# Optimization experiments

Measured on AMD Instinct MI355X. Metric: run time of the kernel, lower is better.

Reference implementation:

```python
import jax, jax.numpy as jnp
import numpy as np

B, P, D, N, H = 1, 256, 512, 8, 64
STD = 0.02
IGNORE = -1000000.0


def setup_inputs() -> dict:
    key = jax.random.key(0)
    ks = jax.random.split(key, 9)
    inp = {"normalized_resid_pre": jax.random.normal(ks[0], (B, P, D), jnp.float32)}
    for i, s in enumerate("ABCDE"):
        inp["W_" + s] = STD * jax.random.normal(ks[i + 1], (N, D, H), jnp.float32)
        inp["b_" + s] = jnp.zeros((N, H), jnp.float32)
    inp["W_V"] = STD * jax.random.normal(ks[6], (N, H, H, H), jnp.float32)
    inp["W_K"] = STD * jax.random.normal(ks[7], (N, H, H, H), jnp.float32)
    inp["W_O"] = STD * jax.random.normal(ks[8], (N, H, D), jnp.float32)
    inp["b_O"] = jnp.zeros((D,), jnp.float32)
    return inp


def reference(normalized_resid_pre, W_A, b_A, W_B, b_B, W_C, b_C, W_D, b_D, W_E, b_E, W_V, W_K, W_O, b_O):
    x = normalized_resid_pre
    b_sz = x.shape[0]
    proj = lambda W, b: jnp.einsum('ndh,bpd->bpnh', W, x) + b
    ta = proj(W_A, b_A)
    tb = proj(W_B, b_B)
    tc = proj(W_C, b_C)
    td = proj(W_D, b_D)
    te = proj(W_E, b_E)
    # V_Layer: v[b, p1, p2, n, h3]
    v = jnp.einsum('bpnh,bqng,nhgf->bpqnf', td, te, W_V)
    # TrittentionCScore: chained einsums -> scores[b, n, p, q, r]
    step1 = jnp.einsum('brnk,nijk->brij', tc, W_K)
    step2 = jnp.einsum('brij,bqnj->briq', step1, tb)
    scores = jnp.einsum('briq,bpni->bnpqr', step2, ta)
    # CausalMask (attn_eq=False, order_attn=True): mask over (t=p, s=q, q=r) dims
    ti = jnp.arange(P)[:, None, None]
    si = jnp.arange(P)[None, :, None]
    qi = jnp.arange(P)[None, None, :]
    mask = (ti >= qi) | (si >= qi) | (ti >= si)  # [P, P, P]
    scores = jnp.where(mask, IGNORE, scores)
    # TrittentionCPattern: b n p q r -> b n r (p q), /d_head, extra column, softmax
    flat = jnp.transpose(scores, (0, 1, 4, 2, 3)).reshape(b_sz, N, P, P * P) / H
    extra = jnp.full((b_sz, N, P, 1), -1000.0, flat.dtype)
    attn = jax.nn.softmax(jnp.concatenate([flat, extra], axis=-1), axis=-1)
    # Z_Layer: v -> b n h (p s), extra zero column, combine
    vf = jnp.transpose(v, (0, 3, 4, 1, 2)).reshape(b_sz, N, H, P * P)
    vf = jnp.concatenate([vf, jnp.zeros((b_sz, N, H, 1), vf.dtype)], axis=-1)
    z = jnp.einsum('bnql,bnhl->bqnh', attn, vf)
    # Result + Out
    zint = jnp.einsum('bqnh,nhd->bqnd', z, W_O)
    return zint.sum(axis=2) + b_O
```

## Files before the change

kernel.cpp:

```cpp
#include <hip/hip_runtime.h>
#include <hip/hip_bf16.h>


typedef __hip_bfloat16 bf16;
typedef __attribute__((ext_vector_type(8))) short short8;
typedef __attribute__((ext_vector_type(4))) short s16x4;
typedef __attribute__((ext_vector_type(4))) float floatx4;

__device__ __forceinline__ float ldf(const float* p){ return *p; }
__device__ __forceinline__ float ldf(const bf16* p){ return __bfloat162float(*p); }
__device__ __forceinline__ void  stf(float* p, float v){ *p = v; }
__device__ __forceinline__ void  stf(bf16*  p, float v){ *p = __float2bfloat16(v); }

__device__ __forceinline__ floatx4 mfma16(short8 a, short8 b, floatx4 c){
  return __builtin_amdgcn_mfma_f32_16x16x32_bf16(a, b, c, 0, 0, 0);
}
__device__ __forceinline__ short8 ld_g8(const bf16* p){
  return *reinterpret_cast<const short8*>(p);
}
__device__ __forceinline__ short bfs(float x){
  bf16 v = __float2bfloat16(x);
  return *reinterpret_cast<short*>(&v);
}

__device__ __forceinline__ void ld4(const bf16* p, float* o){
  s16x4 v = *reinterpret_cast<const s16x4*>(p);
  #pragma unroll
  for (int i = 0; i < 4; i++)
    o[i] = __uint_as_float(((unsigned)(unsigned short)v[i]) << 16);
}
__device__ __forceinline__ void ld4(const float* p, float* o){
  float4 v = *reinterpret_cast<const float4*>(p);
  o[0] = v.x; o[1] = v.y; o[2] = v.z; o[3] = v.w;
}

__device__ __forceinline__ bool is_bf16_x(const void* xv)
{
  const unsigned* x32 = (const unsigned*)xv;
  unsigned w = x32[threadIdx.x & 63];
  unsigned lo = w & 0xFFFFu;
  unsigned e  = (lo >> 7) & 0xFFu;
  bool v = (lo == 0u) || (e >= 90u && e <= 145u);
  unsigned long long m = __ballot(v);
  return __popcll(m) >= 40;
}

template<typename TI>
__device__ __forceinline__ void proj_body(
    const TI* __restrict__ x, const TI* const* Ws, const TI* const* bs,
    bf16* __restrict__ tproj, float* As, float* Bs)
{
  const int bz = blockIdx.z, j = bz >> 3, n = bz & 7;
  const TI* B    = Ws[j] + (size_t)n * 32768;
  const TI* bias = bs[j] + n * 64;
  bf16* out = tproj + (size_t)j * 131072;
  const int m0 = blockIdx.y * 64;
  const int t = threadIdx.x, tx = t & 15, ty = t >> 4;
  float acc[4][4] = {};
  for (int k0 = 0; k0 < 512; k0 += 16) {
    { int m = t >> 2, kk = (t & 3) * 4;
      float a[4]; ld4(x + (size_t)(m0 + m) * 512 + (k0 + kk), a);
      As[(kk+0)*68+m] = a[0]; As[(kk+1)*68+m] = a[1];
      As[(kk+2)*68+m] = a[2]; As[(kk+3)*68+m] = a[3]; }
    { int kk = t >> 4, nn = (t & 15) * 4;
      float b[4]; ld4(B + (size_t)(k0 + kk) * 64 + nn, b);
      Bs[kk*68+nn+0] = b[0]; Bs[kk*68+nn+1] = b[1];
      Bs[kk*68+nn+2] = b[2]; Bs[kk*68+nn+3] = b[3]; }
    __syncthreads();
    #pragma unroll
    for (int kk = 0; kk < 16; kk++) {
      float4 a4 = *reinterpret_cast<const float4*>(&As[kk*68 + ty*4]);
      float4 b4 = *reinterpret_cast<const float4*>(&Bs[kk*68 + tx*4]);
      float av[4] = {a4.x,a4.y,a4.z,a4.w}, bv[4] = {b4.x,b4.y,b4.z,b4.w};
      #pragma unroll
      for (int im = 0; im < 4; im++)
        #pragma unroll
        for (int in = 0; in < 4; in++) acc[im][in] += av[im] * bv[in];
    }
    __syncthreads();
  }
  #pragma unroll
  for (int im = 0; im < 4; im++)
    #pragma unroll
    for (int in = 0; in < 4; in++) {
      float v = acc[im][in] + ldf(bias + tx*4 + in);
      int p = m0 + ty*4 + im, h = tx*4 + in;
      if (j < 3) out[(size_t)p * 512 + n*64 + h] = __float2bfloat16(v);
      else       out[(size_t)n * 16384 + (size_t)h * 256 + p] = __float2bfloat16(v);
    }
}

__global__ __launch_bounds__(256) void proj_all(
    const void* __restrict__ x,
    const void* W0, const void* b0, const void* W1, const void* b1,
    const void* W2, const void* b2, const void* W3, const void* b3,
    const void* W4, const void* b4, bf16* __restrict__ tproj)
{
  __shared__ float As[16*68];
  __shared__ float Bs[16*68];
  if (is_bf16_x(x)) {
    const bf16* Ws[5] = {(const bf16*)W0,(const bf16*)W1,(const bf16*)W2,
                         (const bf16*)W3,(const bf16*)W4};
    const bf16* bs[5] = {(const bf16*)b0,(const bf16*)b1,(const bf16*)b2,
                         (const bf16*)b3,(const bf16*)b4};
    proj_body<bf16>((const bf16*)x, Ws, bs, tproj, As, Bs);
  } else {
    const float* Ws[5] = {(const float*)W0,(const float*)W1,(const float*)W2,
                          (const float*)W3,(const float*)W4};
    const float* bs[5] = {(const float*)b0,(const float*)b1,(const float*)b2,
                          (const float*)b3,(const float*)b4};
    proj_body<float>((const float*)x, Ws, bs, tproj, As, Bs);
  }
}

template<typename TW>
__device__ __forceinline__ void s1t_body(
    const bf16* __restrict__ tc, const TW* __restrict__ WK,
    bf16* __restrict__ s1t)
{
  const int i = blockIdx.x;
  const int t = threadIdx.x, wid = t >> 6, lane = t & 63, quad = lane >> 4, l16 = lane & 15;
  const int rw = blockIdx.y * 64 + wid * 16;
  floatx4 acc[4];
  #pragma unroll
  for (int jt = 0; jt < 4; jt++) acc[jt] = (floatx4){0.f, 0.f, 0.f, 0.f};
  for (int kc = 0; kc < 16; kc++) {
    short8 af = ld_g8(tc + (size_t)(rw + l16) * 512 + kc*32 + quad*8);
    const int n = kc >> 1, kk = (kc & 1) * 32 + quad * 8;
    #pragma unroll
    for (int jt = 0; jt < 4; jt++) {
      const TW* bp = WK + ((size_t)(n*64 + i) * 64 + jt*16 + l16) * 64 + kk;
      short8 bf;
      if constexpr (sizeof(TW) == 2) {
        bf = ld_g8((const bf16*)bp);
      } else {
        float4 x0 = *reinterpret_cast<const float4*>(bp);
        float4 x1 = *reinterpret_cast<const float4*>(bp + 4);
        bf[0]=bfs(x0.x); bf[1]=bfs(x0.y); bf[2]=bfs(x0.z); bf[3]=bfs(x0.w);
        bf[4]=bfs(x1.x); bf[5]=bfs(x1.y); bf[6]=bfs(x1.z); bf[7]=bfs(x1.w);
      }
      acc[jt] = mfma16(af, bf, acc[jt]);
    }
  }
  #pragma unroll
  for (int jt = 0; jt < 4; jt++)
    #pragma unroll
    for (int reg = 0; reg < 4; reg++)
      s1t[(size_t)(rw + quad*4 + reg) * 4096 + i*64 + jt*16 + l16] =
          __float2bfloat16(acc[jt][reg]);
}

__global__ __launch_bounds__(256) void s1t_all(
    const void* __restrict__ x, const bf16* __restrict__ tb,
    const bf16* __restrict__ tc, const void* __restrict__ WK,
    bf16* __restrict__ tbsbf, bf16* __restrict__ s1t)
{
  if (blockIdx.y == 4) {
    int t = blockIdx.x * 256 + threadIdx.x;
    int q = t >> 6, j = t & 63;
    float s = 0.f;
    #pragma unroll
    for (int n = 0; n < 8; n++) s += ldf(tb + q*512 + n*64 + j);
    tbsbf[t] = __float2bfloat16(s * 0.015625f);
    return;
  }
  if (is_bf16_x(x)) s1t_body<bf16>(tc, (const bf16*)WK, s1t);
  else              s1t_body<float>(tc, (const float*)WK, s1t);
}

#define E_PHASE(PT, BUF)                                                      \
  {                                                                           \
    const int ptb_ = ((PT)*4 + wid) * 16;                                     \
    for (int qt2 = 0; qt2 < 2; qt2++) {                                       \
      const int qh = qc + qt2*16;                                             \
      char* erow0 = (BUF) + (quad*4)*72 + (qt2*16 + l16)*2;                   \
      if (qh + 15 <= ptb_) {                                                  \
        for (int reg = 0; reg < 4; reg++)                                     \
          *reinterpret_cast<bf16*>(erow0 + reg*72) = __float2bfloat16(0.f);   \
      } else {                                                                \
        floatx4 acc = {0.f, 0.f, 0.f, 0.f};                                   \
        acc = mfma16(taf[PT][0], cfr[qt2][0], acc);                           \
        acc = mfma16(taf[PT][1], cfr[qt2][1], acc);                           \
        if (qh >= ptb_ + 16 && qh + 15 < r) {                                 \
          for (int reg = 0; reg < 4; reg++) {                                 \
            float e = __expf(acc[reg]);                                       \
            Zp += e;                                                          \
            *reinterpret_cast<bf16*>(erow0 + reg*72) = __float2bfloat16(e);   \
          }                                                                   \
        } else {                                                              \
          for (int reg = 0; reg < 4; reg++) {                                 \
            int p = ptb_ + quad*4 + reg;                                      \
            int q = qh + l16;                                                 \
            float e = (p < q && q < r) ? __expf(acc[reg]) : 0.f;              \
            Zp += e;                                                          \
            *reinterpret_cast<bf16*>(erow0 + reg*72) = __float2bfloat16(e);   \
          }                                                                   \
        }                                                                     \
      }                                                                       \
    }                                                                         \
  }

__global__ __launch_bounds__(256) void tri_attn(
    const bf16* __restrict__ ta,
    const bf16* __restrict__ tbsbf,
    const bf16* __restrict__ s1t,
    const bf16* __restrict__ tdT,
    const bf16* __restrict__ teT,
    bf16* __restrict__ Sbuf)
{
  __shared__ __align__(16) char smb[44544];
  const int bx = blockIdx.x;
  const int n = bx & 7;
  const int r = 255 - (bx >> 3);
  const int t = threadIdx.x;
  const int wid = t >> 6, lane = t & 63, quad = lane >> 4, l16 = lane & 15;
  bf16* srow = Sbuf + (size_t)n * 1048576 + (size_t)r * 4096;
  if (r < 2) {
    short8 zz = (short8){0,0,0,0,0,0,0,0};
    reinterpret_cast<short8*>(srow)[t]       = zz;
    reinterpret_cast<short8*>(srow)[t + 256] = zz;
    return;
  }
  const int nch  = ((r - 1) >> 5) + 1;
  const int rcap = nch * 32;

  {
    const bf16* s1r = s1t + (size_t)r * 4096;
    short8 bfr[4][2];
    #pragma unroll
    for (int it = 0; it < 4; it++)
      #pragma unroll
      for (int kc = 0; kc < 2; kc++)
        bfr[it][kc] = ld_g8(s1r + (it*16 + l16)*64 + kc*32 + quad*8);
    #pragma unroll
    for (int qt = 0; qt < 4; qt++) {
      const int q0 = wid * 64 + qt * 16;
      if (q0 >= rcap) continue;
      if (q0 >= r) {
        #pragma unroll
        for (int it = 0; it < 4; it++)
          #pragma unroll
          for (int reg = 0; reg < 4; reg++) {
            int q = q0 + quad*4 + reg;
            *reinterpret_cast<bf16*>(smb + q*136 + (it*16 + l16)*2) =
                __float2bfloat16(0.f);
          }
        continue;
      }
      short8 af0 = ld_g8(tbsbf + (q0 + l16)*64 + quad*8);
      short8 af1 = ld_g8(tbsbf + (q0 + l16)*64 + 32 + quad*8);
      #pragma unroll
      for (int it = 0; it < 4; it++) {
        floatx4 acc = {0.f, 0.f, 0.f, 0.f};
        acc = mfma16(af0, bfr[it][0], acc);
        acc = mfma16(af1, bfr[it][1], acc);
        #pragma unroll
        for (int reg = 0; reg < 4; reg++) {
          int q = q0 + quad*4 + reg;
          float v = (q >= 1 && q < r) ? acc[reg] : 0.f;
          *reinterpret_cast<bf16*>(smb + q*136 + (it*16 + l16)*2) = __float2bfloat16(v);
        }
      }
    }
  }
  short8 taf[4][2];
  #pragma unroll
  for (int pt = 0; pt < 4; pt++)
    #pragma unroll
    for (int kc = 0; kc < 2; kc++)
      taf[pt][kc] = ld_g8(ta + (size_t)((pt*4 + wid)*16 + l16)*512 + n*64
                             + kc*32 + quad*8);
  __syncthreads();

  floatx4 Tacc[4][4];
  #pragma unroll
  for (int pt = 0; pt < 4; pt++)
    #pragma unroll
    for (int gt = 0; gt < 4; gt++) Tacc[pt][gt] = (floatx4){0.f, 0.f, 0.f, 0.f};
  float Zp = 0.f;
  char* bufA = smb + 34816 + wid * 2304;
  char* bufB = bufA + 1152;
  for (int ch = 0; ch < nch; ch++) {
    const int qc = ch * 32;
    if (qc + 31 <= wid * 16) continue;
    short8 cfr[2][2];
    #pragma unroll
    for (int qt2 = 0; qt2 < 2; qt2++)
      #pragma unroll
      for (int kc = 0; kc < 2; kc++)
        cfr[qt2][kc] = *reinterpret_cast<const short8*>(
            smb + (qc + qt2*16 + l16)*136 + (kc*32 + quad*8)*2);
    short8 tef[4];
    #pragma unroll
    for (int gt = 0; gt < 4; gt++)
      tef[gt] = ld_g8(teT + (size_t)n*16384 + (gt*16 + l16)*256 + qc + quad*8);

    {
      const bool alive0 = ((0*4 + wid)*16 < qc + 31);
      const bool alive1 = ((1*4 + wid)*16 < qc + 31);
      short8 ef0, ef1;
      if (alive0) { E_PHASE(0, bufA)
                    ef0 = *reinterpret_cast<const short8*>(bufA + l16*72 + quad*16); }
      if (alive1) { E_PHASE(1, bufB)
                    ef1 = *reinterpret_cast<const short8*>(bufB + l16*72 + quad*16); }
      if (alive0) { __builtin_amdgcn_s_setprio(1);
        #pragma unroll
        for (int gt = 0; gt < 4; gt++) Tacc[0][gt] = mfma16(ef0, tef[gt], Tacc[0][gt]);
        __builtin_amdgcn_s_setprio(0); }
      if (alive1) { __builtin_amdgcn_s_setprio(1);
        #pragma unroll
        for (int gt = 0; gt < 4; gt++) Tacc[1][gt] = mfma16(ef1, tef[gt], Tacc[1][gt]);
        __builtin_amdgcn_s_setprio(0); }
    }
    {
      const bool alive2 = ((2*4 + wid)*16 < qc + 31);
      const bool alive3 = ((3*4 + wid)*16 < qc + 31);
      short8 ef2, ef3;
      if (alive2) { E_PHASE(2, bufA)
                    ef2 = *reinterpret_cast<const short8*>(bufA + l16*72 + quad*16); }
      if (alive3) { E_PHASE(3, bufB)
                    ef3 = *reinterpret_cast<const short8*>(bufB + l16*72 + quad*16); }
      if (alive2) { __builtin_amdgcn_s_setprio(1);
        #pragma unroll
        for (int gt = 0; gt < 4; gt++) Tacc[2][gt] = mfma16(ef2, tef[gt], Tacc[2][gt]);
        __builtin_amdgcn_s_setprio(0); }
      if (alive3) { __builtin_amdgcn_s_setprio(1);
        #pragma unroll
        for (int gt = 0; gt < 4; gt++) Tacc[3][gt] = mfma16(ef3, tef[gt], Tacc[3][gt]);
        __builtin_amdgcn_s_setprio(0); }
    }
  }
  #pragma unroll
  for (int off = 32; off; off >>= 1) Zp += __shfl_down(Zp, off);
  float* scr = reinterpret_cast<float*>(smb + 44032);
  if (lane == 0) scr[wid] = Zp;
  __syncthreads();
  const float rinv = 1.f / (scr[0] + scr[1] + scr[2] + scr[3]);

  #pragma unroll
  for (int pt = 0; pt < 4; pt++) {
    if ((pt*4 + wid)*16 >= rcap) continue;
    #pragma unroll
    for (int gt = 0; gt < 4; gt++)
      #pragma unroll
      for (int reg = 0; reg < 4; reg++) {
        int g = gt*16 + l16;
        int p = (pt*4 + wid)*16 + quad*4 + reg;
        *reinterpret_cast<bf16*>(smb + g*528 + p*2) = __float2bfloat16(Tacc[pt][gt][reg]);
      }
  }
  __syncthreads();

  {
    short8 Taf[8];
    #pragma unroll
    for (int kc = 0; kc < 8; kc++)
      if (kc < nch)
        Taf[kc] = *reinterpret_cast<const short8*>(
            smb + (wid*16 + l16)*528 + (kc*32 + quad*8)*2);
    #pragma unroll
    for (int ht = 0; ht < 4; ht++) {
      floatx4 acc = {0.f, 0.f, 0.f, 0.f};
      __builtin_amdgcn_s_setprio(1);
      #pragma unroll
      for (int kc = 0; kc < 8; kc++) {
        if (kc < nch) {
          short8 bfragd = ld_g8(tdT + (size_t)n*16384 + (ht*16 + l16)*256 + kc*32 + quad*8);
          acc = mfma16(Taf[kc], bfragd, acc);
        }
      }
      __builtin_amdgcn_s_setprio(0);
      #pragma unroll
      for (int reg = 0; reg < 4; reg++) {
        int g = wid*16 + quad*4 + reg, h = ht*16 + l16;
        srow[h*64 + g] = __float2bfloat16(acc[reg] * rinv);
      }
    }
  }
}

template<typename TW>
__device__ __forceinline__ void z_body(
    const bf16* __restrict__ Sbuf, const TW* __restrict__ WV,
    float* __restrict__ zpart, int kslice, char* lds)
{
  const int rt = blockIdx.x, n = blockIdx.y, ks = blockIdx.z;
  const int t = threadIdx.x, wid = t >> 6, lane = t & 63, quad = lane >> 4, l16 = lane & 15;
  const int rw = rt * 16;
  const int k0 = ks * kslice;
  const TW*  wvn = WV   + (size_t)n * 262144;
  const bf16* sn = Sbuf + (size_t)n * 1048576;
  floatx4 acc = {0.f, 0.f, 0.f, 0.f};
  const int row = t >> 3, f8 = (t & 7) * 8;
  for (int kb = k0; kb < k0 + kslice; kb += 32) {
    { const TW* src = wvn + (size_t)(kb + row) * 64 + f8;
      short sv[8];
      if constexpr (sizeof(TW) == 2) {
        short8 v = ld_g8((const bf16*)src);
        #pragma unroll
        for (int j = 0; j < 8; j++) sv[j] = v[j];
      } else {
        float4 a = *reinterpret_cast<const float4*>(src);
        float4 b = *reinterpret_cast<const float4*>(src + 4);
        sv[0]=bfs(a.x); sv[1]=bfs(a.y); sv[2]=bfs(a.z); sv[3]=bfs(a.w);
        sv[4]=bfs(b.x); sv[5]=bfs(b.y); sv[6]=bfs(b.z); sv[7]=bfs(b.w);
      }
      short* dst = reinterpret_cast<short*>(lds + row*136 + f8*2);
      s16x4 lo = {sv[0],sv[1],sv[2],sv[3]}, hi = {sv[4],sv[5],sv[6],sv[7]};
      *reinterpret_cast<s16x4*>(dst)     = lo;
      *reinterpret_cast<s16x4*>(dst + 4) = hi;
    }
    __syncthreads();
    short8 af = ld_g8(sn + (size_t)(rw + l16) * 4096 + kb + quad*8);
    short8 bfv;
    #pragma unroll
    for (int j = 0; j < 8; j++)
      bfv[j] = *reinterpret_cast<const short*>(
          lds + (quad*8 + j)*136 + (wid*16 + l16)*2);
    acc = mfma16(af, bfv, acc);
    __syncthreads();
  }
  float* zp = zpart + (size_t)ks * 131072;
  #pragma unroll
  for (int reg = 0; reg < 4; reg++)
    zp[(size_t)(rw + quad*4 + reg) * 512 + n*64 + wid*16 + l16] = acc[reg];
}

__global__ __launch_bounds__(256) void z_all(
    const void* __restrict__ x, const bf16* __restrict__ Sbuf,
    const void* __restrict__ WV, float* __restrict__ zpart, int kslice)
{
  __shared__ __align__(16) char lds[32 * 136];
  if (is_bf16_x(x)) z_body<bf16>(Sbuf, (const bf16*)WV, zpart, kslice, lds);
  else              z_body<float>(Sbuf, (const float*)WV, zpart, kslice, lds);
}

__global__ __launch_bounds__(256) void zred_kern(
    const float* __restrict__ zpart, bf16* __restrict__ zbb, int ks)
{
  int idx = blockIdx.x * 256 + threadIdx.x;
  float s = 0.f;
  for (int k = 0; k < ks; k++) s += zpart[(size_t)k * 131072 + idx];
  zbb[idx] = __float2bfloat16(s);
}

template<typename TB, typename TC>
__device__ __forceinline__ void gemm_body(
    const bf16* __restrict__ A, const TB* __restrict__ B, TC* __restrict__ C,
    const TB* __restrict__ bias, float* As, float* Bs)
{
  const int m0 = blockIdx.y * 32, n0 = blockIdx.x * 32;
  const int t = threadIdx.x, tx = t & 15, ty = t >> 4;
  float acc[2][2] = {};
  for (int k0 = 0; k0 < 512; k0 += 16) {
    { int m = t >> 3, kk = (t & 7) * 2;
      const bf16* ap = A + (size_t)(m0 + m) * 512 + (k0 + kk);
      As[(kk+0)*34+m] = ldf(ap+0); As[(kk+1)*34+m] = ldf(ap+1); }
    { int kk = t >> 4, nn = (t & 15) * 2;
      const TB* bp = B + (size_t)(k0 + kk) * 512 + (n0 + nn);
      Bs[kk*34+nn+0] = ldf(bp+0); Bs[kk*34+nn+1] = ldf(bp+1); }
    __syncthreads();
    #pragma unroll
    for (int kk = 0; kk < 16; kk++) {
      float a0 = As[kk*34 + ty*2], a1 = As[kk*34 + ty*2 + 1];
      float b0 = Bs[kk*34 + tx*2], b1 = Bs[kk*34 + tx*2 + 1];
      acc[0][0] += a0*b0; acc[0][1] += a0*b1;
      acc[1][0] += a1*b0; acc[1][1] += a1*b1;
    }
    __syncthreads();
  }
  #pragma unroll
  for (int im = 0; im < 2; im++) {
    TC* cp = C + (size_t)(m0 + ty*2 + im) * 512 + n0 + tx*2;
    #pragma unroll
    for (int in = 0; in < 2; in++) {
      float v = acc[im][in] + ldf(bias + n0 + tx*2 + in);
      stf(cp + in, v);
    }
  }
}

__global__ __launch_bounds__(256) void gemm_all(
    const void* __restrict__ x, const bf16* __restrict__ zbb,
    const void* __restrict__ WO, const void* __restrict__ bO,
    void* __restrict__ out)
{
  __shared__ float As[16*34];
  __shared__ float Bs[16*34];
  if (is_bf16_x(x))
    gemm_body<bf16, bf16>(zbb, (const bf16*)WO, (bf16*)out, (const bf16*)bO, As, Bs);
  else
    gemm_body<float, float>(zbb, (const float*)WO, (float*)out, (const float*)bO, As, Bs);
}

extern "C" void kernel_launch(void* const* d_in, const int* in_sizes, int n_in,
                              void* d_out, int out_size, void* d_ws, size_t ws_size,
                              hipStream_t stream)
{
  (void)in_sizes; (void)n_in; (void)out_size;
  char* wsb = (char*)d_ws;
  bf16* tproj = (bf16*)(wsb + 256);
  bf16* tbsbf = (bf16*)(wsb + 1310976);
  bf16* s1t   = (bf16*)(wsb + 1343744);
  bf16* zbb   = (bf16*)(wsb + 3440896);
  bf16* Sbuf  = (bf16*)(wsb + 4194304);
  const long TE = 131072;
  const bool bigws = (ws_size == 0) || (ws_size >= 25165824);
  const int  ks     = bigws ? 8 : 2;
  const int  kslice = 4096 / ks;
  float* zpart = (float*)(bigws ? (wsb + 20971520) : (wsb + 1343744));

  proj_all<<<dim3(1,4,40), 256, 0, stream>>>(
      d_in[0], d_in[1], d_in[2], d_in[3], d_in[4], d_in[5], d_in[6],
      d_in[7], d_in[8], d_in[9], d_in[10], tproj);
  s1t_all<<<dim3(64,5), 256, 0, stream>>>(
      d_in[0], tproj + 1*TE, tproj + 2*TE, d_in[12], tbsbf, s1t);
  tri_attn<<<2048, 256, 0, stream>>>(
      tproj, tbsbf, s1t, tproj + 3*TE, tproj + 4*TE, Sbuf);
  z_all<<<dim3(16,8,ks), 256, 0, stream>>>(
      d_in[0], Sbuf, d_in[11], zpart, kslice);
  zred_kern<<<512, 256, 0, stream>>>(zpart, zbb, ks);
  gemm_all<<<dim3(16,8), 256, 0, stream>>>(
      d_in[0], zbb, d_in[13], d_in[14], d_out);
}
```

Before: 244.9 us.

## Prefetch next chunk operands in tri_attn and fuse split-K reduction into output GEMM

In the attention kernel, each wave now starts at its first live chunk instead of skipping dead ones, and loads the next chunk's LDS C fragments and global E fragments while computing the current one. This register double-buffering is meant to hide load latency behind MFMA and exp work, at the cost of extra VGPRs. The z kernel now always uses 4 K-slices, and the separate zred reduction kernel is removed. The output GEMM sums the four fp32 partials directly, which saves one launch and the bf16 round trip. The fixed 4-slice split reuses workspace at offset 1343744, overlapping the s1t buffer, which is safe only because s1t is consumed before z_all runs.

After: 300.4 us. +22.7%, slower.

```diff
diff --git a/kernel.cpp b/kernel.cpp
--- a/kernel.cpp
+++ b/kernel.cpp
@@ -179,8 +179,8 @@
           *reinterpret_cast<bf16*>(erow0 + reg*72) = __float2bfloat16(0.f);   \
       } else {                                                                \
         floatx4 acc = {0.f, 0.f, 0.f, 0.f};                                   \
-        acc = mfma16(taf[PT][0], cfr[qt2][0], acc);                           \
-        acc = mfma16(taf[PT][1], cfr[qt2][1], acc);                           \
+        acc = mfma16(taf[PT][0], (qt2 ? cfr10 : cfr00), acc);                 \
+        acc = mfma16(taf[PT][1], (qt2 ? cfr11 : cfr01), acc);                 \
         if (qh >= ptb_ + 16 && qh + 15 < r) {                                 \
           for (int reg = 0; reg < 4; reg++) {                                 \
             float e = __expf(acc[reg]);                                       \
@@ -280,21 +280,37 @@
   float Zp = 0.f;
   char* bufA = smb + 34816 + wid * 2304;
   char* bufB = bufA + 1152;
-  for (int ch = 0; ch < nch; ch++) {
+  const bf16* teTn = teT + (size_t)n * 16384;
+  const int ch0 = wid >> 1;
+
+  short8 cfr00, cfr01, cfr10, cfr11;
+  short8 tef0, tef1, tef2, tef3;
+  if (ch0 < nch) {
+    const int qc = ch0 * 32;
+    cfr00 = *reinterpret_cast<const short8*>(smb + (qc + l16)*136 + (quad*8)*2);
+    cfr01 = *reinterpret_cast<const short8*>(smb + (qc + l16)*136 + (32 + quad*8)*2);
+    cfr10 = *reinterpret_cast<const short8*>(smb + (qc + 16 + l16)*136 + (quad*8)*2);
+    cfr11 = *reinterpret_cast<const short8*>(smb + (qc + 16 + l16)*136 + (32 + quad*8)*2);
+    tef0 = ld_g8(teTn + (0*16 + l16)*256 + qc + quad*8);
+    tef1 = ld_g8(teTn + (1*16 + l16)*256 + qc + quad*8);
+    tef2 = ld_g8(teTn + (2*16 + l16)*256 + qc + quad*8);
+    tef3 = ld_g8(teTn + (3*16 + l16)*256 + qc + quad*8);
+  }
+  for (int ch = ch0; ch < nch; ch++) {
     const int qc = ch * 32;
-    if (qc + 31 <= wid * 16) continue;
-    short8 cfr[2][2];
-    #pragma unroll
-    for (int qt2 = 0; qt2 < 2; qt2++)
-      #pragma unroll
-      for (int kc = 0; kc < 2; kc++)
-        cfr[qt2][kc] = *reinterpret_cast<const short8*>(
-            smb + (qc + qt2*16 + l16)*136 + (kc*32 + quad*8)*2);
-    short8 tef[4];
-    #pragma unroll
-    for (int gt = 0; gt < 4; gt++)
-      tef[gt] = ld_g8(teT + (size_t)n*16384 + (gt*16 + l16)*256 + qc + quad*8);
-
+    short8 ncfr00, ncfr01, ncfr10, ncfr11, ntef0, ntef1, ntef2, ntef3;
+    const bool hasN = (ch + 1 < nch);
+    if (hasN) {
+      const int qn = qc + 32;
+      ncfr00 = *reinterpret_cast<const short8*>(smb + (qn + l16)*136 + (quad*8)*2);
+      ncfr01 = *reinterpret_cast<const short8*>(smb + (qn + l16)*136 + (32 + quad*8)*2);
+      ncfr10 = *reinterpret_cast<const short8*>(smb + (qn + 16 + l16)*136 + (quad*8)*2);
+      ncfr11 = *reinterpret_cast<const short8*>(smb + (qn + 16 + l16)*136 + (32 + quad*8)*2);
+      ntef0 = ld_g8(teTn + (0*16 + l16)*256 + qn + quad*8);
+      ntef1 = ld_g8(teTn + (1*16 + l16)*256 + qn + quad*8);
+      ntef2 = ld_g8(teTn + (2*16 + l16)*256 + qn + quad*8);
+      ntef3 = ld_g8(teTn + (3*16 + l16)*256 + qn + quad*8);
+    }
     {
       const bool alive0 = ((0*4 + wid)*16 < qc + 31);
       const bool alive1 = ((1*4 + wid)*16 < qc + 31);
@@ -304,12 +320,16 @@
       if (alive1) { E_PHASE(1, bufB)
                     ef1 = *reinterpret_cast<const short8*>(bufB + l16*72 + quad*16); }
       if (alive0) { __builtin_amdgcn_s_setprio(1);
-        #pragma unroll
-        for (int gt = 0; gt < 4; gt++) Tacc[0][gt] = mfma16(ef0, tef[gt], Tacc[0][gt]);
+        Tacc[0][0] = mfma16(ef0, tef0, Tacc[0][0]);
+        Tacc[0][1] = mfma16(ef0, tef1, Tacc[0][1]);
+        Tacc[0][2] = mfma16(ef0, tef2, Tacc[0][2]);
+        Tacc[0][3] = mfma16(ef0, tef3, Tacc[0][3]);
         __builtin_amdgcn_s_setprio(0); }
       if (alive1) { __builtin_amdgcn_s_setprio(1);
-        #pragma unroll
-        for (int gt = 0; gt < 4; gt++) Tacc[1][gt] = mfma16(ef1, tef[gt], Tacc[1][gt]);
+        Tacc[1][0] = mfma16(ef1, tef0, Tacc[1][0]);
+        Tacc[1][1] = mfma16(ef1, tef1, Tacc[1][1]);
+        Tacc[1][2] = mfma16(ef1, tef2, Tacc[1][2]);
+        Tacc[1][3] = mfma16(ef1, tef3, Tacc[1][3]);
         __builtin_amdgcn_s_setprio(0); }
     }
     {
@@ -321,13 +341,21 @@
       if (alive3) { E_PHASE(3, bufB)
                     ef3 = *reinterpret_cast<const short8*>(bufB + l16*72 + quad*16); }
       if (alive2) { __builtin_amdgcn_s_setprio(1);
-        #pragma unroll
-        for (int gt = 0; gt < 4; gt++) Tacc[2][gt] = mfma16(ef2, tef[gt], Tacc[2][gt]);
+        Tacc[2][0] = mfma16(ef2, tef0, Tacc[2][0]);
+        Tacc[2][1] = mfma16(ef2, tef1, Tacc[2][1]);
+        Tacc[2][2] = mfma16(ef2, tef2, Tacc[2][2]);
+        Tacc[2][3] = mfma16(ef2, tef3, Tacc[2][3]);
         __builtin_amdgcn_s_setprio(0); }
       if (alive3) { __builtin_amdgcn_s_setprio(1);
-        #pragma unroll
-        for (int gt = 0; gt < 4; gt++) Tacc[3][gt] = mfma16(ef3, tef[gt], Tacc[3][gt]);
+        Tacc[3][0] = mfma16(ef3, tef0, Tacc[3][0]);
+        Tacc[3][1] = mfma16(ef3, tef1, Tacc[3][1]);
+        Tacc[3][2] = mfma16(ef3, tef2, Tacc[3][2]);
+        Tacc[3][3] = mfma16(ef3, tef3, Tacc[3][3]);
         __builtin_amdgcn_s_setprio(0); }
+    }
+    if (hasN) {
+      cfr00 = ncfr00; cfr01 = ncfr01; cfr10 = ncfr10; cfr11 = ncfr11;
+      tef0 = ntef0; tef1 = ntef1; tef2 = ntef2; tef3 = ntef3;
     }
   }
   #pragma unroll
@@ -435,18 +463,9 @@
   else              z_body<float>(Sbuf, (const float*)WV, zpart, kslice, lds);
 }
 
-__global__ __launch_bounds__(256) void zred_kern(
-    const float* __restrict__ zpart, bf16* __restrict__ zbb, int ks)
-{
-  int idx = blockIdx.x * 256 + threadIdx.x;
-  float s = 0.f;
-  for (int k = 0; k < ks; k++) s += zpart[(size_t)k * 131072 + idx];
-  zbb[idx] = __float2bfloat16(s);
-}
-
 template<typename TB, typename TC>
 __device__ __forceinline__ void gemm_body(
-    const bf16* __restrict__ A, const TB* __restrict__ B, TC* __restrict__ C,
+    const float* __restrict__ zp, const TB* __restrict__ B, TC* __restrict__ C,
     const TB* __restrict__ bias, float* As, float* Bs)
 {
   const int m0 = blockIdx.y * 32, n0 = blockIdx.x * 32;
@@ -454,8 +473,13 @@
   float acc[2][2] = {};
   for (int k0 = 0; k0 < 512; k0 += 16) {
     { int m = t >> 3, kk = (t & 7) * 2;
-      const bf16* ap = A + (size_t)(m0 + m) * 512 + (k0 + kk);
-      As[(kk+0)*34+m] = ldf(ap+0); As[(kk+1)*34+m] = ldf(ap+1); }
+      size_t base = (size_t)(m0 + m) * 512 + (k0 + kk);
+      float2 u0 = *reinterpret_cast<const float2*>(zp + base);
+      float2 u1 = *reinterpret_cast<const float2*>(zp + 131072 + base);
+      float2 u2 = *reinterpret_cast<const float2*>(zp + 262144 + base);
+      float2 u3 = *reinterpret_cast<const float2*>(zp + 393216 + base);
+      As[(kk+0)*34+m] = u0.x + u1.x + u2.x + u3.x;
+      As[(kk+1)*34+m] = u0.y + u1.y + u2.y + u3.y; }
     { int kk = t >> 4, nn = (t & 15) * 2;
       const TB* bp = B + (size_t)(k0 + kk) * 512 + (n0 + nn);
       Bs[kk*34+nn+0] = ldf(bp+0); Bs[kk*34+nn+1] = ldf(bp+1); }
@@ -481,34 +505,30 @@
 }
 
 __global__ __launch_bounds__(256) void gemm_all(
-    const void* __restrict__ x, const bf16* __restrict__ zbb,
+    const void* __restrict__ x, const float* __restrict__ zpart,
     const void* __restrict__ WO, const void* __restrict__ bO,
     void* __restrict__ out)
 {
   __shared__ float As[16*34];
   __shared__ float Bs[16*34];
   if (is_bf16_x(x))
-    gemm_body<bf16, bf16>(zbb, (const bf16*)WO, (bf16*)out, (const bf16*)bO, As, Bs);
+    gemm_body<bf16, bf16>(zpart, (const bf16*)WO, (bf16*)out, (const bf16*)bO, As, Bs);
   else
-    gemm_body<float, float>(zbb, (const float*)WO, (float*)out, (const float*)bO, As, Bs);
+    gemm_body<float, float>(zpart, (const float*)WO, (float*)out, (const float*)bO, As, Bs);
 }
 
 extern "C" void kernel_launch(void* const* d_in, const int* in_sizes, int n_in,
                               void* d_out, int out_size, void* d_ws, size_t ws_size,
                               hipStream_t stream)
 {
-  (void)in_sizes; (void)n_in; (void)out_size;
+  (void)in_sizes; (void)n_in; (void)out_size; (void)ws_size;
   char* wsb = (char*)d_ws;
   bf16* tproj = (bf16*)(wsb + 256);
   bf16* tbsbf = (bf16*)(wsb + 1310976);
   bf16* s1t   = (bf16*)(wsb + 1343744);
-  bf16* zbb   = (bf16*)(wsb + 3440896);
+  float* zpart = (float*)(wsb + 1343744);
   bf16* Sbuf  = (bf16*)(wsb + 4194304);
   const long TE = 131072;
-  const bool bigws = (ws_size == 0) || (ws_size >= 25165824);
-  const int  ks     = bigws ? 8 : 2;
-  const int  kslice = 4096 / ks;
-  float* zpart = (float*)(bigws ? (wsb + 20971520) : (wsb + 1343744));
 
   proj_all<<<dim3(1,4,40), 256, 0, stream>>>(
       d_in[0], d_in[1], d_in[2], d_in[3], d_in[4], d_in[5], d_in[6],
@@ -517,9 +537,8 @@
       d_in[0], tproj + 1*TE, tproj + 2*TE, d_in[12], tbsbf, s1t);
   tri_attn<<<2048, 256, 0, stream>>>(
       tproj, tbsbf, s1t, tproj + 3*TE, tproj + 4*TE, Sbuf);
-  z_all<<<dim3(16,8,ks), 256, 0, stream>>>(
-      d_in[0], Sbuf, d_in[11], zpart, kslice);
-  zred_kern<<<512, 256, 0, stream>>>(zpart, zbb, ks);
+  z_all<<<dim3(16,8,4), 256, 0, stream>>>(
+      d_in[0], Sbuf, d_in[11], zpart, 1024);
   gemm_all<<<dim3(16,8), 256, 0, stream>>>(
-      d_in[0], zbb, d_in[13], d_in[14], d_out);
-}
+      d_in[0], zpart, d_in[13], d_in[14], d_out);
+}
```

## Double tri_attn block to 512 threads and split tiles across eight waves

Applied to the files above, without the earlier changes.

Launches the triple-attention kernel with eight waves per block instead of four. Each wave now owns two p-tiles rather than four, and half of the head tiles in the final product. LDS grows to hold per-wave exp buffers and an eight-entry partial-sum scratch. The aim is more latency hiding per block and fewer accumulator registers per wave. In exchange, larger blocks and more LDS per block could lower the number of resident blocks and add sync cost.

Result: slower. 256.7 us (+4.8%).

```diff
diff --git a/kernel.cpp b/kernel.cpp
--- a/kernel.cpp
+++ b/kernel.cpp
@@ -170,7 +170,7 @@
 
 #define E_PHASE(PT, BUF)                                                      \
   {                                                                           \
-    const int ptb_ = ((PT)*4 + wid) * 16;                                     \
+    const int ptb_ = ((PT)*8 + wid) * 16;                                     \
     for (int qt2 = 0; qt2 < 2; qt2++) {                                       \
       const int qh = qc + qt2*16;                                             \
       char* erow0 = (BUF) + (quad*4)*72 + (qt2*16 + l16)*2;                   \
@@ -200,7 +200,7 @@
     }                                                                         \
   }
 
-__global__ __launch_bounds__(256) void tri_attn(
+__global__ __launch_bounds__(512) void tri_attn(
     const bf16* __restrict__ ta,
     const bf16* __restrict__ tbsbf,
     const bf16* __restrict__ s1t,
@@ -208,7 +208,7 @@
     const bf16* __restrict__ teT,
     bf16* __restrict__ Sbuf)
 {
-  __shared__ __align__(16) char smb[44544];
+  __shared__ __align__(16) char smb[53760];
   const int bx = blockIdx.x;
   const int n = bx & 7;
   const int r = 255 - (bx >> 3);
@@ -217,8 +217,7 @@
   bf16* srow = Sbuf + (size_t)n * 1048576 + (size_t)r * 4096;
   if (r < 2) {
     short8 zz = (short8){0,0,0,0,0,0,0,0};
-    reinterpret_cast<short8*>(srow)[t]       = zz;
-    reinterpret_cast<short8*>(srow)[t + 256] = zz;
+    reinterpret_cast<short8*>(srow)[t] = zz;
     return;
   }
   const int nch  = ((r - 1) >> 5) + 1;
@@ -233,8 +232,8 @@
       for (int kc = 0; kc < 2; kc++)
         bfr[it][kc] = ld_g8(s1r + (it*16 + l16)*64 + kc*32 + quad*8);
     #pragma unroll
-    for (int qt = 0; qt < 4; qt++) {
-      const int q0 = wid * 64 + qt * 16;
+    for (int qt = 0; qt < 2; qt++) {
+      const int q0 = wid * 32 + qt * 16;
       if (q0 >= rcap) continue;
       if (q0 >= r) {
         #pragma unroll
@@ -263,18 +262,18 @@
       }
     }
   }
-  short8 taf[4][2];
-  #pragma unroll
-  for (int pt = 0; pt < 4; pt++)
+  short8 taf[2][2];
+  #pragma unroll
+  for (int pt = 0; pt < 2; pt++)
     #pragma unroll
     for (int kc = 0; kc < 2; kc++)
-      taf[pt][kc] = ld_g8(ta + (size_t)((pt*4 + wid)*16 + l16)*512 + n*64
+      taf[pt][kc] = ld_g8(ta + (size_t)((pt*8 + wid)*16 + l16)*512 + n*64
                              + kc*32 + quad*8);
   __syncthreads();
 
-  floatx4 Tacc[4][4];
-  #pragma unroll
-  for (int pt = 0; pt < 4; pt++)
+  floatx4 Tacc[2][4];
+  #pragma unroll
+  for (int pt = 0; pt < 2; pt++)
     #pragma unroll
     for (int gt = 0; gt < 4; gt++) Tacc[pt][gt] = (floatx4){0.f, 0.f, 0.f, 0.f};
   float Zp = 0.f;
@@ -295,71 +294,56 @@
     for (int gt = 0; gt < 4; gt++)
       tef[gt] = ld_g8(teT + (size_t)n*16384 + (gt*16 + l16)*256 + qc + quad*8);
 
-    {
-      const bool alive0 = ((0*4 + wid)*16 < qc + 31);
-      const bool alive1 = ((1*4 + wid)*16 < qc + 31);
-      short8 ef0, ef1;
-      if (alive0) { E_PHASE(0, bufA)
-                    ef0 = *reinterpret_cast<const short8*>(bufA + l16*72 + quad*16); }
-      if (alive1) { E_PHASE(1, bufB)
-                    ef1 = *reinterpret_cast<const short8*>(bufB + l16*72 + quad*16); }
-      if (alive0) { __builtin_amdgcn_s_setprio(1);
-        #pragma unroll
-        for (int gt = 0; gt < 4; gt++) Tacc[0][gt] = mfma16(ef0, tef[gt], Tacc[0][gt]);
-        __builtin_amdgcn_s_setprio(0); }
-      if (alive1) { __builtin_amdgcn_s_setprio(1);
-        #pragma unroll
-        for (int gt = 0; gt < 4; gt++) Tacc[1][gt] = mfma16(ef1, tef[gt], Tacc[1][gt]);
-        __builtin_amdgcn_s_setprio(0); }
-    }
-    {
-      const bool alive2 = ((2*4 + wid)*16 < qc + 31);
-      const bool alive3 = ((3*4 + wid)*16 < qc + 31);
-      short8 ef2, ef3;
-      if (alive2) { E_PHASE(2, bufA)
-                    ef2 = *reinterpret_cast<const short8*>(bufA + l16*72 + quad*16); }
-      if (alive3) { E_PHASE(3, bufB)
-                    ef3 = *reinterpret_cast<const short8*>(bufB + l16*72 + quad*16); }
-      if (alive2) { __builtin_amdgcn_s_setprio(1);
-        #pragma unroll
-        for (int gt = 0; gt < 4; gt++) Tacc[2][gt] = mfma16(ef2, tef[gt], Tacc[2][gt]);
-        __builtin_amdgcn_s_setprio(0); }
-      if (alive3) { __builtin_amdgcn_s_setprio(1);
-        #pragma unroll
-        for (int gt = 0; gt < 4; gt++) Tacc[3][gt] = mfma16(ef3, tef[gt], Tacc[3][gt]);
-        __builtin_amdgcn_s_setprio(0); }
-    }
+    const bool alive1 = (((1*8 + wid)*16) < qc + 31);
+    short8 ef0, ef1;
+    E_PHASE(0, bufA)
+    ef0 = *reinterpret_cast<const short8*>(bufA + l16*72 + quad*16);
+    if (alive1) { E_PHASE(1, bufB)
+                  ef1 = *reinterpret_cast<const short8*>(bufB + l16*72 + quad*16); }
+    __builtin_amdgcn_s_setprio(1);
+    #pragma unroll
+    for (int gt = 0; gt < 4; gt++) Tacc[0][gt] = mfma16(ef0, tef[gt], Tacc[0][gt]);
+    __builtin_amdgcn_s_setprio(0);
+    if (alive1) { __builtin_amdgcn_s_setprio(1);
+      #pragma unroll
+      for (int gt = 0; gt < 4; gt++) Tacc[1][gt] = mfma16(ef1, tef[gt], Tacc[1][gt]);
+      __builtin_amdgcn_s_setprio(0); }
   }
   #pragma unroll
   for (int off = 32; off; off >>= 1) Zp += __shfl_down(Zp, off);
-  float* scr = reinterpret_cast<float*>(smb + 44032);
+  float* scr = reinterpret_cast<float*>(smb + 53248);
   if (lane == 0) scr[wid] = Zp;
   __syncthreads();
-  const float rinv = 1.f / (scr[0] + scr[1] + scr[2] + scr[3]);
-
-  #pragma unroll
-  for (int pt = 0; pt < 4; pt++) {
-    if ((pt*4 + wid)*16 >= rcap) continue;
+  const float rinv = 1.f / (scr[0] + scr[1] + scr[2] + scr[3] +
+                            scr[4] + scr[5] + scr[6] + scr[7]);
+
+  #pragma unroll
+  for (int pt = 0; pt < 2; pt++) {
+    if ((pt*8 + wid)*16 >= rcap) continue;
     #pragma unroll
     for (int gt = 0; gt < 4; gt++)
       #pragma unroll
       for (int reg = 0; reg < 4; reg++) {
         int g = gt*16 + l16;
-        int p = (pt*4 + wid)*16 + quad*4 + reg;
+        int p = (pt*8 + wid)*16 + quad*4 + reg;
         *reinterpret_cast<bf16*>(smb + g*528 + p*2) = __float2bfloat16(Tacc[pt][gt][reg]);
       }
   }
   __syncthreads();
 
   {
+    const int gq = wid & 3, hh = wid >> 1 & 2;
+    const int hbase = (wid >> 2) * 2;
+    (void)hh;
     short8 Taf[8];
     #pragma unroll
     for (int kc = 0; kc < 8; kc++)
       if (kc < nch)
         Taf[kc] = *reinterpret_cast<const short8*>(
-            smb + (wid*16 + l16)*528 + (kc*32 + quad*8)*2);
-    #pragma unroll
-    for (int ht = 0; ht < 4; ht++) {
+            smb + (gq*16 + l16)*528 + (kc*32 + quad*8)*2);
+    #pragma unroll
+    for (int hl = 0; hl < 2; hl++) {
+      const int ht = hbase + hl;
       floatx4 acc = {0.f, 0.f, 0.f, 0.f};
       __builtin_amdgcn_s_setprio(1);
       #pragma unroll
@@ -372,7 +356,7 @@
       __builtin_amdgcn_s_setprio(0);
       #pragma unroll
       for (int reg = 0; reg < 4; reg++) {
-        int g = wid*16 + quad*4 + reg, h = ht*16 + l16;
+        int g = gq*16 + quad*4 + reg, h = ht*16 + l16;
         srow[h*64 + g] = __float2bfloat16(acc[reg] * rinv);
       }
     }
@@ -515,7 +499,7 @@
       d_in[7], d_in[8], d_in[9], d_in[10], tproj);
   s1t_all<<<dim3(64,5), 256, 0, stream>>>(
       d_in[0], tproj + 1*TE, tproj + 2*TE, d_in[12], tbsbf, s1t);
-  tri_attn<<<2048, 256, 0, stream>>>(
+  tri_attn<<<2048, 512, 0, stream>>>(
       tproj, tbsbf, s1t, tproj + 3*TE, tproj + 4*TE, Sbuf);
   z_all<<<dim3(16,8,ks), 256, 0, stream>>>(
       d_in[0], Sbuf, d_in[11], zpart, kslice);
```
